# Kernel optimization log

Measured on AMD Instinct MI355X. Metric: run time of the kernel, lower is better.

Reference implementation:

```python
import jax, jax.numpy as jnp
import numpy as np

B, S, T, H, V = 32, 64, 64, 512, 32000


def setup_inputs() -> dict:
    key = jax.random.key(0)
    ks = jax.random.split(key, 14)
    enc = jax.random.normal(ks[0], (B, S, H), jnp.float32)
    h0 = jax.random.normal(ks[1], (1, B, H), jnp.float32)
    # encoder padding mask: at least half of each row valid (avoids all -inf rows)
    src_len = jax.random.randint(ks[2], (B,), S // 2, S + 1)
    enc_mask = (jnp.arange(S)[None, :] < src_len[:, None])
    tgt = jax.random.randint(ks[3], (B, T), 0, V)
    fra_len = jax.random.randint(ks[4], (B,), 1, T + 1).at[0].set(T)
    s = 1.0 / np.sqrt(H)
    emb = jax.random.normal(ks[5], (V, H), jnp.float32) * s
    W_ih = jax.random.uniform(ks[6], (3 * H, H), jnp.float32, -s, s)
    W_hh = jax.random.uniform(ks[7], (3 * H, H), jnp.float32, -s, s)
    b_ih = jax.random.uniform(ks[8], (3 * H,), jnp.float32, -s, s)
    b_hh = jax.random.uniform(ks[9], (3 * H,), jnp.float32, -s, s)
    W_cc = jax.random.uniform(ks[10], (H, 2 * H), jnp.float32, -s, s)
    b_cc = jnp.zeros((H,), jnp.float32)
    W_out = jax.random.uniform(ks[11], (V, H), jnp.float32, -s, s)
    b_out = jnp.zeros((V,), jnp.float32)
    return {"all_encoder_hidden_states": enc, "initial_decoder_hidden_state": h0,
            "encoder_output_mask": enc_mask, "target_input": tgt, "fra_length": fra_len,
            "embedding": emb, "W_ih": W_ih, "W_hh": W_hh, "b_ih": b_ih, "b_hh": b_hh,
            "W_cc": W_cc, "b_cc": b_cc, "W_out": W_out, "b_out": b_out}


def reference(all_encoder_hidden_states, initial_decoder_hidden_state, encoder_output_mask,
              target_input, fra_length, embedding, W_ih, W_hh, b_ih, b_hh,
              W_cc, b_cc, W_out, b_out):
    enc = all_encoder_hidden_states            # [B,S,H]
    mask = encoder_output_mask                 # [B,S] bool
    xs = embedding[target_input].transpose(1, 0, 2)  # [T,B,H]
    ts = jnp.arange(xs.shape[0])

    def step(h, inp):                          # h: [B,H]
        x, t = inp
        gx = x @ W_ih.T + b_ih                 # [B,3H]
        gh = h @ W_hh.T + b_hh
        gxr, gxz, gxn = jnp.split(gx, 3, axis=-1)
        ghr, ghz, ghn = jnp.split(gh, 3, axis=-1)
        r = jax.nn.sigmoid(gxr + ghr)
        z = jax.nn.sigmoid(gxz + ghz)
        n = jnp.tanh(gxn + r * ghn)
        h_new = (1.0 - z) * n + z * h          # torch GRU update
        # Luong dot-product attention
        scores = jnp.einsum('bsh,bh->bs', enc, h_new)
        scores = jnp.where(mask, scores, -jnp.inf)
        alphas = jax.nn.softmax(scores, axis=-1)
        ctx = jnp.einsum('bs,bsh->bh', alphas, enc)
        ho = jnp.tanh(jnp.concatenate([ctx, h_new], axis=-1) @ W_cc.T + b_cc)
        logit = ho @ W_out.T + b_out           # [B,V]
        active = (t < fra_length)[:, None]
        h_next = jnp.where(active, h_new, h)   # freeze finished sequences
        return h_next, logit

    _, logits = jax.lax.scan(step, initial_decoder_hidden_state[0], (xs, ts))
    logits = logits.transpose(1, 0, 2)          # [B,T,V]
    return jax.nn.log_softmax(logits, axis=-1)
```

## Files before the change

kernel.cpp:

```cpp
#include <hip/hip_runtime.h>

static constexpr int Bn = 32, Sn = 64, Tn = 64, Hn = 512, Vn = 32000;
static constexpr int H3 = 1536;

typedef __attribute__((ext_vector_type(8))) short bf16x8;
typedef __attribute__((ext_vector_type(4))) float f32x4;

__device__ __forceinline__ short f2bf(float f) {
    unsigned u = __float_as_uint(f);
    u += 0x7FFFu + ((u >> 16) & 1u);
    return (short)(u >> 16);
}
__device__ __forceinline__ float bf2f(short s) {
    return __uint_as_float(((unsigned)(unsigned short)s) << 16);
}

__device__ __forceinline__ void gload16(const void* g, void* l) {
    __builtin_amdgcn_global_load_lds(
        (const __attribute__((address_space(1))) unsigned int*)g,
        (__attribute__((address_space(3))) unsigned int*)l, 16, 0, 0);
}

__global__ __launch_bounds__(256) void k_prep(const int* __restrict__ tgt,
                                              const float* __restrict__ emb,
                                              const float* __restrict__ W_ih,
                                              const float* __restrict__ W_hh,
                                              const float* __restrict__ W_cc,
                                              short* __restrict__ Xb,
                                              short* __restrict__ Wih_b, short* __restrict__ Whh_b,
                                              short* __restrict__ Wc1_b, short* __restrict__ Wc2_b) {
    const int bid = blockIdx.x, tid = threadIdx.x;
    if (bid < 2048) {
        long u = (long)bid * 256 + tid;
        const float* src; short* dst;
        if (u < 196608)       { long e = u * 4;            src = W_ih + e; dst = Wih_b + e; }
        else if (u < 393216)  { long e = (u - 196608) * 4; src = W_hh + e; dst = Whh_b + e; }
        else if (u < 458752)  { long e = (u - 393216) * 4; long r = e >> 9; int c = (int)(e & 511);
                                src = W_cc + r * 1024 + c;       dst = Wc1_b + e; }
        else                  { long e = (u - 458752) * 4; long r = e >> 9; int c = (int)(e & 511);
                                src = W_cc + r * 1024 + 512 + c; dst = Wc2_b + e; }
        const float4 v = *(const float4*)src;
        short4 o; o.x = f2bf(v.x); o.y = f2bf(v.y); o.z = f2bf(v.z); o.w = f2bf(v.w);
        *(short4*)dst = o;
    } else {
        const int m = (bid - 2048) * 2 + (tid >> 7);
        const int c = (tid & 127) * 4;
        const float4 v = *(const float4*)(emb + (long)tgt[m] * Hn + c);
        short4 o; o.x = f2bf(v.x); o.y = f2bf(v.y); o.z = f2bf(v.z); o.w = f2bf(v.w);
        *(short4*)(Xb + (long)m * Hn + c) = o;
    }
}

__global__ __launch_bounds__(256) void k_gemm_bf16(const short* __restrict__ A, int lda,
                                                   const short* __restrict__ Bm, int ldb,
                                                   const float* __restrict__ bias,
                                                   float* __restrict__ C, int ldc, int K) {
    __shared__ short lA[4096];
    __shared__ short lB[4096];
    const int tid = threadIdx.x;
    const int row0 = blockIdx.y * 128;
    const int col0 = blockIdx.x * 128;
    const int lane = tid & 63;
    const int w = tid >> 6;
    const int wr = w >> 1, wc = w & 1;
    const int g = lane >> 4, rr = lane & 15;

    f32x4 acc[4][4];
    for (int m = 0; m < 4; ++m)
        for (int n = 0; n < 4; ++n)
            for (int q = 0; q < 4; ++q) acc[m][n][q] = 0.f;

    for (int kk = 0; kk < K; kk += 32) {
        for (int p = 0; p < 2; ++p) {
            int u = p * 256 + tid;
            int kg = u >> 7, r = u & 127;
            gload16(A + (long)(row0 + r) * lda + kk + kg * 8, &lA[u * 8]);
            gload16(Bm + (long)(col0 + r) * ldb + kk + kg * 8, &lB[u * 8]);
        }
        __syncthreads();
        bf16x8 av[4], bv[4];
        for (int m = 0; m < 4; ++m)
            av[m] = *(const bf16x8*)&lA[(g * 128 + wr * 64 + m * 16 + rr) * 8];
        for (int n = 0; n < 4; ++n)
            bv[n] = *(const bf16x8*)&lB[(g * 128 + wc * 64 + n * 16 + rr) * 8];
        for (int m = 0; m < 4; ++m)
            for (int n = 0; n < 4; ++n)
                acc[m][n] = __builtin_amdgcn_mfma_f32_16x16x32_bf16(av[m], bv[n], acc[m][n], 0, 0, 0);
        __syncthreads();
    }

    for (int n = 0; n < 4; ++n) {
        int gc = col0 + wc * 64 + n * 16 + rr;
        float bb = bias ? bias[gc] : 0.f;
        for (int m = 0; m < 4; ++m) {
            int gr = row0 + wr * 64 + m * 16 + g * 4;
            for (int q = 0; q < 4; ++q)
                C[(long)(gr + q) * ldc + gc] = acc[m][n][q] + bb;
        }
    }
}

__global__ __launch_bounds__(256) void k_gemm_logits(const short* __restrict__ A,
                                                     const short* __restrict__ Bm,
                                                     const float* __restrict__ bias,
                                                     float* __restrict__ Cf,
                                                     short* __restrict__ Cb,
                                                     float* __restrict__ stats,
                                                     int use_bf16) {
    __shared__ short lA[4096];
    __shared__ short lB[4096];
    __shared__ float sml[128][2];
    __shared__ float ssl[128][2];
    const int tid = threadIdx.x;
    const int ctile = blockIdx.x >> 4;
    const int row0 = (blockIdx.x & 15) * 128;
    const int col0 = ctile * 128;
    const int lane = tid & 63;
    const int w = tid >> 6;
    const int wr = w >> 1, wc = w & 1;
    const int g = lane >> 4, rr = lane & 15;

    f32x4 acc[4][4];
    for (int m = 0; m < 4; ++m)
        for (int n = 0; n < 4; ++n)
            for (int q = 0; q < 4; ++q) acc[m][n][q] = 0.f;

    for (int kk = 0; kk < 512; kk += 32) {
        for (int p = 0; p < 2; ++p) {
            int u = p * 256 + tid;
            int kg = u >> 7, r = u & 127;
            gload16(A + (long)(row0 + r) * 512 + kk + kg * 8, &lA[u * 8]);
            gload16(Bm + (long)(col0 + r) * 512 + kk + kg * 8, &lB[u * 8]);
        }
        __syncthreads();
        bf16x8 av[4], bv[4];
        for (int m = 0; m < 4; ++m)
            av[m] = *(const bf16x8*)&lA[(g * 128 + wr * 64 + m * 16 + rr) * 8];
        for (int n = 0; n < 4; ++n)
            bv[n] = *(const bf16x8*)&lB[(g * 128 + wc * 64 + n * 16 + rr) * 8];
        for (int m = 0; m < 4; ++m)
            for (int n = 0; n < 4; ++n)
                acc[m][n] = __builtin_amdgcn_mfma_f32_16x16x32_bf16(av[m], bv[n], acc[m][n], 0, 0, 0);
        __syncthreads();
    }

    float bb[4];
    #pragma unroll
    for (int n = 0; n < 4; ++n) bb[n] = bias[col0 + wc * 64 + n * 16 + rr];

    if (use_bf16) {
        #pragma unroll
        for (int n = 0; n < 4; ++n) {
            int gc = col0 + wc * 64 + n * 16 + rr;
            #pragma unroll
            for (int m = 0; m < 4; ++m) {
                int gr = row0 + wr * 64 + m * 16 + g * 4;
                #pragma unroll
                for (int q = 0; q < 4; ++q)
                    Cb[(long)(gr + q) * Vn + gc] = f2bf(acc[m][n][q] + bb[n]);
            }
        }
    } else {
        #pragma unroll
        for (int n = 0; n < 4; ++n) {
            int gc = col0 + wc * 64 + n * 16 + rr;
            #pragma unroll
            for (int m = 0; m < 4; ++m) {
                int gr = row0 + wr * 64 + m * 16 + g * 4;
                #pragma unroll
                for (int q = 0; q < 4; ++q)
                    Cf[(long)(gr + q) * Vn + gc] = acc[m][n][q] + bb[n];
            }
        }
    }
    #pragma unroll
    for (int m = 0; m < 4; ++m) {
        #pragma unroll
        for (int q = 0; q < 4; ++q) {
            float mx = acc[m][0][q] + bb[0];
            mx = fmaxf(mx, acc[m][1][q] + bb[1]);
            mx = fmaxf(mx, acc[m][2][q] + bb[2]);
            mx = fmaxf(mx, acc[m][3][q] + bb[3]);
            mx = fmaxf(mx, __shfl_xor(mx, 1));
            mx = fmaxf(mx, __shfl_xor(mx, 2));
            mx = fmaxf(mx, __shfl_xor(mx, 4));
            mx = fmaxf(mx, __shfl_xor(mx, 8));
            float s = __expf(acc[m][0][q] + bb[0] - mx) + __expf(acc[m][1][q] + bb[1] - mx)
                    + __expf(acc[m][2][q] + bb[2] - mx) + __expf(acc[m][3][q] + bb[3] - mx);
            s += __shfl_xor(s, 1);
            s += __shfl_xor(s, 2);
            s += __shfl_xor(s, 4);
            s += __shfl_xor(s, 8);
            if (rr == 0) {
                const int r = wr * 64 + m * 16 + g * 4 + q;
                sml[r][wc] = mx; ssl[r][wc] = s;
            }
        }
    }
    __syncthreads();
    if (tid < 128) {
        const float m0 = sml[tid][0], m1 = sml[tid][1];
        const float mm = fmaxf(m0, m1);
        const float ss = ssl[tid][0] * __expf(m0 - mm) + ssl[tid][1] * __expf(m1 - mm);
        float2* sp = (float2*)stats;
        sp[(long)(row0 + tid) * 256 + ctile] = make_float2(mm, ss);
    }
}

__global__ __launch_bounds__(256) void k_sub(float* __restrict__ out, const short* __restrict__ Cb,
                                             const float* __restrict__ stats, int use_bf16) {
    const long row = blockIdx.x;
    const int tid = threadIdx.x;
    __shared__ float lse_s;
    if (tid < 64) {
        float m = -__builtin_inff(), s = 0.f;
        for (int tc = tid; tc < 250; tc += 64) {
            const float2 p = ((const float2*)stats)[row * 256 + tc];
            const float nm = fmaxf(m, p.x);
            s = s * __expf(m - nm) + p.y * __expf(p.x - nm);
            m = nm;
        }
        for (int o = 1; o < 64; o <<= 1) {
            const float om = __shfl_xor(m, o), os = __shfl_xor(s, o);
            const float nm = fmaxf(m, om);
            s = s * __expf(m - nm) + os * __expf(om - nm);
            m = nm;
        }
        if (tid == 0) lse_s = m + logf(s);
    }
    __syncthreads();
    const float lse = lse_s;
    float* p = out + row * (long)Vn;
    if (use_bf16) {
        const short* cp = Cb + row * (long)Vn;
        for (int i = tid; i < Vn / 4; i += 256) {
            short4 c = *(const short4*)(cp + i * 4);
            float4 v;
            v.x = bf2f(c.x) - lse; v.y = bf2f(c.y) - lse;
            v.z = bf2f(c.z) - lse; v.w = bf2f(c.w) - lse;
            *(float4*)(p + i * 4) = v;
        }
    } else {
        for (int i = tid; i < Vn / 4; i += 256) {
            float4 v = *(const float4*)(p + i * 4);
            v.x -= lse; v.y -= lse; v.z -= lse; v.w -= lse;
            *(float4*)(p + i * 4) = v;
        }
    }
}

__global__ __launch_bounds__(256) void k_ho(const short* __restrict__ A1, const short* __restrict__ A2,
                                            const short* __restrict__ B1, const short* __restrict__ B2,
                                            const float* __restrict__ bias, short* __restrict__ C) {
    __shared__ short lA[4096];
    __shared__ short lB[4096];
    const int tid = threadIdx.x;
    const int row0 = blockIdx.y * 128;
    const int col0 = blockIdx.x * 128;
    const int lane = tid & 63;
    const int w = tid >> 6;
    const int wr = w >> 1, wc = w & 1;
    const int g = lane >> 4, rr = lane & 15;

    f32x4 acc[4][4];
    for (int m = 0; m < 4; ++m)
        for (int n = 0; n < 4; ++n)
            for (int q = 0; q < 4; ++q) acc[m][n][q] = 0.f;

    for (int ph = 0; ph < 2; ++ph) {
        const short* A = ph ? A2 : A1;
        const short* Bm = ph ? B2 : B1;
        for (int kk = 0; kk < 512; kk += 32) {
            for (int p = 0; p < 2; ++p) {
                int u = p * 256 + tid;
                int kg = u >> 7, r = u & 127;
                gload16(A + (long)(row0 + r) * 512 + kk + kg * 8, &lA[u * 8]);
                gload16(Bm + (long)(col0 + r) * 512 + kk + kg * 8, &lB[u * 8]);
            }
            __syncthreads();
            bf16x8 av[4], bv[4];
            for (int m = 0; m < 4; ++m)
                av[m] = *(const bf16x8*)&lA[(g * 128 + wr * 64 + m * 16 + rr) * 8];
            for (int n = 0; n < 4; ++n)
                bv[n] = *(const bf16x8*)&lB[(g * 128 + wc * 64 + n * 16 + rr) * 8];
            for (int m = 0; m < 4; ++m)
                for (int n = 0; n < 4; ++n)
                    acc[m][n] = __builtin_amdgcn_mfma_f32_16x16x32_bf16(av[m], bv[n], acc[m][n], 0, 0, 0);
            __syncthreads();
        }
    }

    for (int n = 0; n < 4; ++n) {
        int gc = col0 + wc * 64 + n * 16 + rr;
        float bb = bias[gc];
        for (int m = 0; m < 4; ++m) {
            int gr = row0 + wr * 64 + m * 16 + g * 4;
            for (int q = 0; q < 4; ++q)
                C[(long)(gr + q) * 512 + gc] = f2bf(tanhf(acc[m][n][q] + bb));
        }
    }
}

__device__ __forceinline__ void sig_flag(unsigned* slot, unsigned val) {
    asm volatile("s_waitcnt vmcnt(0)" ::: "memory");
    __syncthreads();
    if (threadIdx.x == 0)
        __hip_atomic_store(slot, val, __ATOMIC_RELAXED, __HIP_MEMORY_SCOPE_AGENT);
}
__device__ __forceinline__ void wait_flags32(const unsigned* base, unsigned need) {
    if (threadIdx.x < 32) {
        while (__hip_atomic_load(base + threadIdx.x * 32, __ATOMIC_RELAXED, __HIP_MEMORY_SCOPE_AGENT) < need)
            __builtin_amdgcn_s_sleep(1);
    }
    __syncthreads();
}

__global__ __launch_bounds__(512, 1) void k_seq(
    const float* __restrict__ GX, const int* __restrict__ fra,
    const float* __restrict__ h0,
    const short* __restrict__ Whh_b, const float* __restrict__ b_hh,
    short* __restrict__ hn_all,
    unsigned long long* __restrict__ hn_pub,
    unsigned* __restrict__ flags,
    const float* __restrict__ W_out, short* __restrict__ Wout_b)
{
    __shared__ __align__(16) short h_all[Bn * Hn];
    __shared__ float gh_sl[3 * 16 * 32];
    const int bid = blockIdx.x;
    const int tid = threadIdx.x;

    if (bid >= Bn) {
        const long base = (long)(bid - Bn) * (512 * 16);
        #pragma unroll
        for (int it = 0; it < 16; ++it) {
            long i = base + it * 512 + tid;
            if (i < (long)Vn * Hn / 4) {
                const float4 v = *(const float4*)(W_out + i * 4);
                short4 o; o.x = f2bf(v.x); o.y = f2bf(v.y); o.z = f2bf(v.z); o.w = f2bf(v.w);
                *(short4*)(Wout_b + i * 4) = o;
            }
        }
        return;
    }

    const int wv = tid >> 6, lane = tid & 63;
    bf16x8 afr[16];
    if (wv < 6) {
        const int g = wv >> 1;
        const int row = g * 512 + bid * 16 + (lane & 15);
        #pragma unroll
        for (int k = 0; k < 16; ++k)
            afr[k] = *(const bf16x8*)(Whh_b + (long)row * 512 + k * 32 + (lane >> 4) * 8);
    }
    #pragma unroll
    for (int it = 0; it < 8; ++it) {
        const int idx2 = it * 512 + tid;
        const int b = idx2 >> 7, ci2 = idx2 & 127;
        const int j0 = ci2 * 4;
        const int soff = b * 512 + ((((ci2 >> 1)) ^ (b & 7)) << 3) + (ci2 & 1) * 4;
        const float4 v = *(const float4*)(h0 + b * 512 + j0);
        unsigned long long pk = (unsigned long long)(unsigned short)f2bf(v.x)
                              | ((unsigned long long)(unsigned short)f2bf(v.y) << 16)
                              | ((unsigned long long)(unsigned short)f2bf(v.z) << 32)
                              | ((unsigned long long)(unsigned short)f2bf(v.w) << 48);
        *(unsigned long long*)&h_all[soff] = pk;
    }

    const int eb = tid >> 4, jj = tid & 15;
    float h_carry = h0[eb * 512 + bid * 16 + jj];
    const int flen_e = fra[eb];
    const int jglob = bid * 16 + jj;
    const float bhr = b_hh[jglob];
    const float bhz = b_hh[512 + jglob];
    const float bhn = b_hh[1024 + jglob];

    const int ci2s = wv * 16 + (lane & 15);
    const unsigned* fp = flags + (ci2s >> 2) * 32;
    const int bbase = lane >> 4;

    for (int t = 0; t < Tn; ++t) {
        const long base = (long)(eb * Tn + t) * H3 + jglob;
        const float gxr = GX[base];
        const float gxz = GX[base + 512];
        const float gxn = GX[base + 1024];
        if (t >= 1) {
            while (__hip_atomic_load(fp, __ATOMIC_RELAXED, __HIP_MEMORY_SCOPE_AGENT) < (unsigned)t)
                __builtin_amdgcn_s_sleep(1);
            const unsigned long long* src = hn_pub + ((t - 1) & 1) * 4096;
            #pragma unroll
            for (int it = 0; it < 8; ++it) {
                const int b = bbase + it * 4;
                const unsigned long long v =
                    __hip_atomic_load(src + b * 128 + ci2s, __ATOMIC_RELAXED, __HIP_MEMORY_SCOPE_AGENT);
                const int soff = b * 512 + ((((ci2s >> 1)) ^ (b & 7)) << 3) + (ci2s & 1) * 4;
                *(unsigned long long*)&h_all[soff] = v;
            }
        }
        __syncthreads();
        if (wv < 6) {
            const int g = wv >> 1, n = wv & 1;
            const int bq = n * 16 + (lane & 15);
            f32x4 a0 = {0.f, 0.f, 0.f, 0.f}, a1 = {0.f, 0.f, 0.f, 0.f};
            #pragma unroll
            for (int k = 0; k < 8; ++k) {
                const int c0 = k * 4 + (lane >> 4);
                const int c1 = (k + 8) * 4 + (lane >> 4);
                bf16x8 b0 = *(const bf16x8*)&h_all[bq * 512 + ((c0 ^ (bq & 7)) << 3)];
                bf16x8 b1 = *(const bf16x8*)&h_all[bq * 512 + ((c1 ^ (bq & 7)) << 3)];
                a0 = __builtin_amdgcn_mfma_f32_16x16x32_bf16(afr[k], b0, a0, 0, 0, 0);
                a1 = __builtin_amdgcn_mfma_f32_16x16x32_bf16(afr[k + 8], b1, a1, 0, 0, 0);
            }
            const int r0 = (lane >> 4) * 4;
            #pragma unroll
            for (int q = 0; q < 4; ++q)
                gh_sl[g * 512 + (r0 + q) * 32 + bq] = a0[q] + a1[q];
        }
        __syncthreads();
        {
            const float ghr = gh_sl[jj * 32 + eb]          + bhr;
            const float ghz = gh_sl[512 + jj * 32 + eb]    + bhz;
            const float ghn = gh_sl[1024 + jj * 32 + eb]   + bhn;
            const float r = 1.f / (1.f + __expf(-(gxr + ghr)));
            const float z = 1.f / (1.f + __expf(-(gxz + ghz)));
            const float nn = tanhf(gxn + r * ghn);
            const float hv = (1.f - z) * nn + z * h_carry;
            h_carry = (t < flen_e) ? hv : h_carry;
            int w32 = (int)(unsigned short)f2bf(h_carry);
            int n1 = __shfl_down(w32, 1);
            int n2 = __shfl_down(w32, 2);
            int n3 = __shfl_down(w32, 3);
            if ((jj & 3) == 0) {
                unsigned long long pk = (unsigned long long)(unsigned)(w32 | (n1 << 16))
                                      | ((unsigned long long)(unsigned)(n2 | (n3 << 16)) << 32);
                __hip_atomic_store(hn_pub + (t & 1) * 4096 + eb * 128 + bid * 4 + (jj >> 2), pk,
                                   __ATOMIC_RELAXED, __HIP_MEMORY_SCOPE_AGENT);
            }
            sig_flag(flags + bid * 32, (unsigned)(t + 1));
            hn_all[(long)(eb * Tn + t) * Hn + jglob] = f2bf(hv);
        }
    }
}

__global__ __launch_bounds__(512, 1) void k_attn(
    const float* __restrict__ enc, const short* __restrict__ hn_all,
    const void* __restrict__ maskp, short* __restrict__ ctx_b)
{
    __shared__ __align__(16) short encl[64 * 536];
    __shared__ __align__(16) short hnlbuf[64 * 536];
    __shared__ __align__(16) float scl[64 * 64];
    __shared__ __align__(16) short albc[64 * 72];
    const int b = blockIdx.x;
    const int tid = threadIdx.x;
    const int wv = tid >> 6, lane = tid & 63;
    const int g = lane >> 4, rr = lane & 15;

    const unsigned w0 = ((const unsigned*)maskp)[0];
    const int mmode = (w0 == 1u) ? 0 : (w0 == 0x3F800000u ? 2 : 1);

    {
        const float* encb = enc + (long)b * (Sn * Hn);
        #pragma unroll
        for (int it = 0; it < 16; ++it) {
            int e = (it * 512 + tid) * 4;
            float4 v = *(const float4*)(encb + e);
            int s = e >> 9, k = e & 511;
            short4 o; o.x = f2bf(v.x); o.y = f2bf(v.y); o.z = f2bf(v.z); o.w = f2bf(v.w);
            *(short4*)(encl + s * 536 + k) = o;
        }
    }
    {
        const short* hb = hn_all + (long)b * (Tn * Hn);
        #pragma unroll
        for (int it = 0; it < 8; ++it) {
            int u = it * 512 + tid;
            int t = u >> 6, k8 = (u & 63) * 8;
            *(int4*)(hnlbuf + t * 536 + k8) = *(const int4*)(hb + t * 512 + k8);
        }
    }
    __syncthreads();

    for (int i = 0; i < 2; ++i) {
        const int id = wv * 2 + i;
        const int tt = id >> 2, ss = id & 3;
        f32x4 a0 = {0.f, 0.f, 0.f, 0.f}, a1 = {0.f, 0.f, 0.f, 0.f};
        #pragma unroll
        for (int k = 0; k < 8; ++k) {
            bf16x8 av0 = *(const bf16x8*)&hnlbuf[(tt * 16 + rr) * 536 + k * 32 + g * 8];
            bf16x8 bv0 = *(const bf16x8*)&encl[(ss * 16 + rr) * 536 + k * 32 + g * 8];
            bf16x8 av1 = *(const bf16x8*)&hnlbuf[(tt * 16 + rr) * 536 + (k + 8) * 32 + g * 8];
            bf16x8 bv1 = *(const bf16x8*)&encl[(ss * 16 + rr) * 536 + (k + 8) * 32 + g * 8];
            a0 = __builtin_amdgcn_mfma_f32_16x16x32_bf16(av0, bv0, a0, 0, 0, 0);
            a1 = __builtin_amdgcn_mfma_f32_16x16x32_bf16(av1, bv1, a1, 0, 0, 0);
        }
        #pragma unroll
        for (int q = 0; q < 4; ++q)
            scl[(tt * 16 + g * 4 + q) * 64 + ss * 16 + rr] = a0[q] + a1[q];
    }
    __syncthreads();

    {
        const int t = wv * 8 + (lane >> 3);
        const int sub = lane & 7;
        float v[8];
        #pragma unroll
        for (int e = 0; e < 8; ++e) {
            const int s = sub * 8 + e;
            bool mv;
            if (mmode == 0)      mv = ((const int*)maskp)[b * Sn + s] != 0;
            else if (mmode == 1) mv = ((const unsigned char*)maskp)[b * Sn + s] != 0;
            else                 mv = ((const float*)maskp)[b * Sn + s] != 0.f;
            v[e] = mv ? scl[t * 64 + s] : -__builtin_inff();
        }
        float mx = v[0];
        #pragma unroll
        for (int e = 1; e < 8; ++e) mx = fmaxf(mx, v[e]);
        mx = fmaxf(mx, __shfl_xor(mx, 1));
        mx = fmaxf(mx, __shfl_xor(mx, 2));
        mx = fmaxf(mx, __shfl_xor(mx, 4));
        float su = 0.f;
        float ev[8];
        #pragma unroll
        for (int e = 0; e < 8; ++e) { ev[e] = __expf(v[e] - mx); su += ev[e]; }
        su += __shfl_xor(su, 1);
        su += __shfl_xor(su, 2);
        su += __shfl_xor(su, 4);
        const float inv = 1.f / su;
        bf16x8 o;
        #pragma unroll
        for (int e = 0; e < 8; ++e) o[e] = f2bf(ev[e] * inv);
        *(bf16x8*)&albc[t * 72 + sub * 8] = o;
    }
    {
        short* enct = hnlbuf;
        const int j = tid;
        #pragma unroll
        for (int c = 0; c < 8; ++c) {
            bf16x8 tmp;
            #pragma unroll
            for (int e = 0; e < 8; ++e) tmp[e] = encl[(c * 8 + e) * 536 + j];
            *(bf16x8*)&enct[j * 64 + ((c ^ (j & 7)) * 8)] = tmp;
        }
    }
    __syncthreads();

    {
        const short* enct = hnlbuf;
        for (int i = 0; i < 16; ++i) {
            const int id = wv * 16 + i;
            const int tt = id >> 5, jt = id & 31;
            const int jr = jt * 16 + rr;
            f32x4 acc = {0.f, 0.f, 0.f, 0.f};
            #pragma unroll
            for (int kk = 0; kk < 2; ++kk) {
                bf16x8 av = *(const bf16x8*)&albc[(tt * 16 + rr) * 72 + kk * 32 + g * 8];
                const int c = kk * 4 + g;
                bf16x8 bv = *(const bf16x8*)&enct[jr * 64 + ((c ^ (jr & 7)) * 8)];
                acc = __builtin_amdgcn_mfma_f32_16x16x32_bf16(av, bv, acc, 0, 0, 0);
            }
            #pragma unroll
            for (int q = 0; q < 4; ++q) {
                const int t = tt * 16 + g * 4 + q;
                ctx_b[(long)(b * Tn + t) * Hn + jr] = f2bf(acc[q]);
            }
        }
    }
}

extern "C" void kernel_launch(void* const* d_in, const int* in_sizes, int n_in,
                              void* d_out, int out_size, void* d_ws, size_t ws_size,
                              hipStream_t stream) {
    const float* enc   = (const float*)d_in[0];
    const float* h0    = (const float*)d_in[1];
    const void*  maskp = d_in[2];
    const int*   tgt   = (const int*)d_in[3];
    const int*   fra   = (const int*)d_in[4];
    const float* emb   = (const float*)d_in[5];
    const float* W_ih  = (const float*)d_in[6];
    const float* W_hh  = (const float*)d_in[7];
    const float* b_ih  = (const float*)d_in[8];
    const float* b_hh  = (const float*)d_in[9];
    const float* W_cc  = (const float*)d_in[10];
    const float* b_cc  = (const float*)d_in[11];
    const float* W_out = (const float*)d_in[12];
    const float* b_out = (const float*)d_in[13];
    float* out = (float*)d_out;

    char* ws = (char*)d_ws;
    float*    GX      = (float*)ws;   ws += (long)2048 * 1536 * 4;
    short*    Xb      = (short*)ws;   ws += (long)2048 * 512 * 2;
    short*    Wih_b   = (short*)ws;   ws += (long)1536 * 512 * 2;
    short*    Wout_b  = (short*)ws;   ws += (long)32000 * 512 * 2;
    short*    Whh_b   = (short*)ws;   ws += (long)1536 * 512 * 2;
    short*    Wc1_b   = (short*)ws;   ws += (long)512 * 512 * 2;
    short*    Wcc2_b  = (short*)ws;   ws += (long)512 * 512 * 2;
    short*    ho_b    = (short*)ws;   ws += (long)2048 * 512 * 2;
    short*    hn_all  = (short*)ws;   ws += (long)2048 * 512 * 2;
    short*    ctx_b   = (short*)ws;   ws += (long)2048 * 512 * 2;
    float*    stats   = (float*)ws;   ws += (long)2048 * 256 * 2 * 4;
    unsigned long long* hn_pub = (unsigned long long*)ws; ws += (long)2 * 4096 * 8;
    unsigned* flags   = (unsigned*)ws; ws += 1024 * 4;
    const long cb_bytes = (long)2048 * Vn * 2;
    const long used = (long)(ws - (char*)d_ws);
    const int use_bf16 = (ws_size >= (size_t)(used + cb_bytes)) ? 1 : 0;
    short* Cb = use_bf16 ? (short*)ws : nullptr;

    hipMemsetAsync(flags, 0, 1024 * 4, stream);
    k_prep<<<3072, 256, 0, stream>>>(tgt, emb, W_ih, W_hh, W_cc, Xb, Wih_b, Whh_b, Wc1_b, Wcc2_b);

    k_gemm_bf16<<<dim3(12, 16), 256, 0, stream>>>(Xb, 512, Wih_b, 512, b_ih, GX, 1536, 512);

    k_seq<<<544, 512, 0, stream>>>(GX, fra, h0, Whh_b, b_hh, hn_all, hn_pub, flags, W_out, Wout_b);

    k_attn<<<32, 512, 0, stream>>>(enc, hn_all, maskp, ctx_b);

    k_ho<<<dim3(4, 16), 256, 0, stream>>>(ctx_b, hn_all, Wc1_b, Wcc2_b, b_cc, ho_b);

    k_gemm_logits<<<4000, 256, 0, stream>>>(ho_b, Wout_b, b_out, out, Cb, stats, use_bf16);

    k_sub<<<2048, 256, 0, stream>>>(out, Cb, stats, use_bf16);
}
```

Measured before the change: 665.5 us.

## Replace per-block flag barriers with step-tagged hidden-state words in GRU recurrence

Measured after the change: 688.5 us. +3.5%, slower.

```diff
diff --git a/kernel.cpp b/kernel.cpp
--- a/kernel.cpp
+++ b/kernel.cpp
@@ -301,27 +301,12 @@
     }
 }
 
-__device__ __forceinline__ void sig_flag(unsigned* slot, unsigned val) {
-    asm volatile("s_waitcnt vmcnt(0)" ::: "memory");
-    __syncthreads();
-    if (threadIdx.x == 0)
-        __hip_atomic_store(slot, val, __ATOMIC_RELAXED, __HIP_MEMORY_SCOPE_AGENT);
-}
-__device__ __forceinline__ void wait_flags32(const unsigned* base, unsigned need) {
-    if (threadIdx.x < 32) {
-        while (__hip_atomic_load(base + threadIdx.x * 32, __ATOMIC_RELAXED, __HIP_MEMORY_SCOPE_AGENT) < need)
-            __builtin_amdgcn_s_sleep(1);
-    }
-    __syncthreads();
-}
-
 __global__ __launch_bounds__(512, 1) void k_seq(
     const float* __restrict__ GX, const int* __restrict__ fra,
     const float* __restrict__ h0,
     const short* __restrict__ Whh_b, const float* __restrict__ b_hh,
     short* __restrict__ hn_all,
-    unsigned long long* __restrict__ hn_pub,
-    unsigned* __restrict__ flags,
+    unsigned long long* __restrict__ hn_pub2,
     const float* __restrict__ W_out, short* __restrict__ Wout_b)
 {
     __shared__ __align__(16) short h_all[Bn * Hn];
@@ -374,26 +359,37 @@
     const float bhz = b_hh[512 + jglob];
     const float bhn = b_hh[1024 + jglob];
 
-    const int ci2s = wv * 16 + (lane & 15);
-    const unsigned* fp = flags + (ci2s >> 2) * 32;
-    const int bbase = lane >> 4;
-
     for (int t = 0; t < Tn; ++t) {
         const long base = (long)(eb * Tn + t) * H3 + jglob;
         const float gxr = GX[base];
         const float gxz = GX[base + 512];
         const float gxn = GX[base + 1024];
         if (t >= 1) {
-            while (__hip_atomic_load(fp, __ATOMIC_RELAXED, __HIP_MEMORY_SCOPE_AGENT) < (unsigned)t)
+            const unsigned tagv = (unsigned)t;
+            const unsigned long long* src = hn_pub2 + ((t - 1) & 1) * 8192;
+            unsigned long long v[16];
+            #pragma unroll
+            for (int it = 0; it < 16; ++it)
+                v[it] = __hip_atomic_load(src + it * 512 + tid, __ATOMIC_RELAXED, __HIP_MEMORY_SCOPE_AGENT);
+            unsigned pending;
+            for (;;) {
+                pending = 0;
+                #pragma unroll
+                for (int it = 0; it < 16; ++it)
+                    if ((unsigned)(v[it] >> 32) != tagv) pending |= 1u << it;
+                if (!pending) break;
                 __builtin_amdgcn_s_sleep(1);
-            const unsigned long long* src = hn_pub + ((t - 1) & 1) * 4096;
-            #pragma unroll
-            for (int it = 0; it < 8; ++it) {
-                const int b = bbase + it * 4;
-                const unsigned long long v =
-                    __hip_atomic_load(src + b * 128 + ci2s, __ATOMIC_RELAXED, __HIP_MEMORY_SCOPE_AGENT);
-                const int soff = b * 512 + ((((ci2s >> 1)) ^ (b & 7)) << 3) + (ci2s & 1) * 4;
-                *(unsigned long long*)&h_all[soff] = v;
+                #pragma unroll
+                for (int it = 0; it < 16; ++it)
+                    if ((pending >> it) & 1u)
+                        v[it] = __hip_atomic_load(src + it * 512 + tid, __ATOMIC_RELAXED, __HIP_MEMORY_SCOPE_AGENT);
+            }
+            #pragma unroll
+            for (int it = 0; it < 16; ++it) {
+                const int idx = it * 512 + tid;
+                const int b = idx >> 8, pr = idx & 255;
+                const int soff = b * 512 + (((pr >> 2) ^ (b & 7)) << 3) + ((pr >> 1) & 1) * 4 + (pr & 1) * 2;
+                *(unsigned*)&h_all[soff] = (unsigned)v[it];
             }
         }
         __syncthreads();
@@ -425,17 +421,14 @@
             const float nn = tanhf(gxn + r * ghn);
             const float hv = (1.f - z) * nn + z * h_carry;
             h_carry = (t < flen_e) ? hv : h_carry;
-            int w32 = (int)(unsigned short)f2bf(h_carry);
-            int n1 = __shfl_down(w32, 1);
-            int n2 = __shfl_down(w32, 2);
-            int n3 = __shfl_down(w32, 3);
-            if ((jj & 3) == 0) {
-                unsigned long long pk = (unsigned long long)(unsigned)(w32 | (n1 << 16))
-                                      | ((unsigned long long)(unsigned)(n2 | (n3 << 16)) << 32);
-                __hip_atomic_store(hn_pub + (t & 1) * 4096 + eb * 128 + bid * 4 + (jj >> 2), pk,
+            int hb = (int)(unsigned short)f2bf(h_carry);
+            int hb1 = __shfl_down(hb, 1);
+            if (!(jj & 1)) {
+                unsigned long long pk = (unsigned long long)(unsigned)(hb | (hb1 << 16))
+                                      | ((unsigned long long)(unsigned)(t + 1) << 32);
+                __hip_atomic_store(hn_pub2 + (t & 1) * 8192 + eb * 256 + (jglob >> 1), pk,
                                    __ATOMIC_RELAXED, __HIP_MEMORY_SCOPE_AGENT);
             }
-            sig_flag(flags + bid * 32, (unsigned)(t + 1));
             hn_all[(long)(eb * Tn + t) * Hn + jglob] = f2bf(hv);
         }
     }
@@ -597,19 +590,18 @@
     short*    hn_all  = (short*)ws;   ws += (long)2048 * 512 * 2;
     short*    ctx_b   = (short*)ws;   ws += (long)2048 * 512 * 2;
     float*    stats   = (float*)ws;   ws += (long)2048 * 256 * 2 * 4;
-    unsigned long long* hn_pub = (unsigned long long*)ws; ws += (long)2 * 4096 * 8;
-    unsigned* flags   = (unsigned*)ws; ws += 1024 * 4;
+    unsigned long long* hn_pub2 = (unsigned long long*)ws; ws += (long)2 * 8192 * 8;
     const long cb_bytes = (long)2048 * Vn * 2;
     const long used = (long)(ws - (char*)d_ws);
     const int use_bf16 = (ws_size >= (size_t)(used + cb_bytes)) ? 1 : 0;
     short* Cb = use_bf16 ? (short*)ws : nullptr;
 
-    hipMemsetAsync(flags, 0, 1024 * 4, stream);
+    hipMemsetAsync(hn_pub2, 0, 2 * 8192 * 8, stream);
     k_prep<<<3072, 256, 0, stream>>>(tgt, emb, W_ih, W_hh, W_cc, Xb, Wih_b, Whh_b, Wc1_b, Wcc2_b);
 
     k_gemm_bf16<<<dim3(12, 16), 256, 0, stream>>>(Xb, 512, Wih_b, 512, b_ih, GX, 1536, 512);
 
-    k_seq<<<544, 512, 0, stream>>>(GX, fra, h0, Whh_b, b_hh, hn_all, hn_pub, flags, W_out, Wout_b);
+    k_seq<<<544, 512, 0, stream>>>(GX, fra, h0, Whh_b, b_hh, hn_all, hn_pub2, W_out, Wout_b);
 
     k_attn<<<32, 512, 0, stream>>>(enc, hn_all, maskp, ctx_b);
 
```
